# Kernel tuning notes

Hardware: AMD Instinct MI355X
Metric: run time of the kernel (lower is better)

Reference implementation:

```python
import jax, jax.numpy as jnp
import numpy as np
from jax import lax

DIM = 8          # per-head dim
HEADS = 32       # in_channels // dim * heads_ratio = 256 // 8
SCALE = 5        # multi-scale aggregation kernel
EPS = 1e-15


def _conv2d(x, w, groups=1, pad=0):
    # NCHW conv, stride 1, symmetric padding, no bias
    return lax.conv_general_dilated(
        x, w, window_strides=(1, 1), padding=[(pad, pad), (pad, pad)],
        dimension_numbers=('NCHW', 'OIHW', 'NCHW'), feature_group_count=groups)


def setup_inputs() -> dict:
    key = jax.random.key(0)
    ks = jax.random.split(key, 5)
    B, C, H, W = 8, 256, 64, 64
    td = HEADS * DIM                      # total_dim = 256
    x = jax.random.normal(ks[0], (B, C, H, W), jnp.float32)
    w_qkv = jax.random.normal(ks[1], (3 * td, C, 1, 1), jnp.float32) * 0.05
    w_dw = jax.random.normal(ks[2], (3 * td, 1, SCALE, SCALE), jnp.float32) * 0.05
    w_pw = jax.random.normal(ks[3], (3 * td, (3 * td) // (3 * HEADS), 1, 1), jnp.float32) * 0.1
    w_proj = jax.random.normal(ks[4], (C, td * 2, 1, 1), jnp.float32) * 0.05
    return {'x': x, 'w_qkv': w_qkv, 'w_dw': w_dw, 'w_pw': w_pw, 'w_proj': w_proj}


def reference(x, w_qkv, w_dw, w_pw, w_proj):
    B, C, H, W = x.shape
    td = HEADS * DIM
    # qkv projection (1x1 conv, no norm/activation)
    qkv = _conv2d(x, w_qkv)                                        # [B, 3*td, H, W]
    # multi-scale aggregation: depthwise 5x5 then grouped 1x1 (groups = 3*heads)
    agg = _conv2d(qkv, w_dw, groups=3 * td, pad=SCALE // 2)        # depthwise
    agg = _conv2d(agg, w_pw, groups=3 * HEADS)                     # grouped pointwise
    ms = jnp.concatenate([qkv, agg], axis=1)                       # [B, 2*3*td, H, W]
    # reshape to head-groups: [B, G, N, 3*dim] with G = 2*heads, N = H*W
    ms = ms.reshape(B, -1, 3 * DIM, H * W).transpose(0, 1, 3, 2)
    q, k, v = jnp.split(ms, 3, axis=-1)                            # each [B, G, N, d]
    q = jax.nn.relu(q)
    k = jax.nn.relu(k)
    v = jnp.pad(v, ((0, 0), (0, 0), (0, 0), (0, 1)), constant_values=1.0)  # [B,G,N,d+1]
    # linear attention in fp32 (inputs already fp32)
    kv = jnp.einsum('bgnd,bgne->bgde', k, v)                       # [B,G,d,d+1]
    out = jnp.einsum('bgnd,bgde->bgne', q, kv)                     # [B,G,N,d+1]
    out = out[..., :-1] / (out[..., -1:] + EPS)                    # [B,G,N,d]
    out = out.transpose(0, 1, 3, 2).reshape(B, -1, H, W)           # [B, 2*td, H, W]
    return _conv2d(out, w_proj)                                    # [B, C_out, H, W]
```

## Files before the change

kernel.cpp:

```cpp
#include <hip/hip_runtime.h>

#define N_PIX 4096
#define IMG_W 64
#define C_IN 256
#define TD3 768
#define N_B 8
#define N_G 64
#define C_OUT 256

typedef _Float16 f16;
typedef _Float16 half8 __attribute__((ext_vector_type(8)));
typedef _Float16 f16x4 __attribute__((ext_vector_type(4)));
typedef float f32x4 __attribute__((ext_vector_type(4)));

__global__ __launch_bounds__(256) void k_cvtw(const float* __restrict__ wq,
                                              const float* __restrict__ wp,
                                              f16* __restrict__ wqq_h,
                                              f16* __restrict__ wqq_l,
                                              f16* __restrict__ wqkv,
                                              f16* __restrict__ wph) {
  const int i = blockIdx.x * 256 + threadIdx.x;
  if (i < TD3 * C_IN) {
    const int r = i >> 8, k = i & 255;
    const float v = wq[i];
    const f16 h = (f16)v;
    const int g = r / 24, j = r % 24;
    if (j < 8) {
      const int qi = g * 8 + j;
      wqq_h[qi * 256 + k] = h;
      wqq_l[qi * 256 + k] = (f16)(v - (float)h);
    } else {
      const int kvi = g * 16 + (j - 8);
      wqkv[kvi * 256 + k] = h;
    }
  } else if (i < TD3 * C_IN + C_OUT * 512) {
    const int j = i - TD3 * C_IN;
    wph[j] = (f16)wp[j];
  }
}

__global__ __launch_bounds__(256) void k_xT(const float* __restrict__ x,
                                            f16* __restrict__ xh,
                                            f16* __restrict__ xl) {
  __shared__ float st[64][65];
  const int t = threadIdx.x;
  const int n0 = blockIdx.x * 64;
  const int k0 = blockIdx.y * 64;
  const size_t b = blockIdx.z;
  const float* xb = x + b * (size_t)C_IN * N_PIX;
#pragma unroll
  for (int i = 0; i < 16; ++i) {
    const int idx = t + i * 256;
    const int r = idx >> 6, c = idx & 63;
    st[r][c] = xb[(size_t)(k0 + r) * N_PIX + n0 + c];
  }
  __syncthreads();
#pragma unroll
  for (int i = 0; i < 16; ++i) {
    const int idx = t + i * 256;
    const int n = idx >> 6, k = idx & 63;
    const float v = st[k][n];
    const f16 h = (f16)v;
    const size_t o = (b * N_PIX + n0 + n) * C_IN + k0 + k;
    xh[o] = h;
    xl[o] = (f16)(v - (float)h);
  }
}

__global__ __launch_bounds__(256) void k_gemmq(const f16* __restrict__ Ah,
                                               const f16* __restrict__ Al,
                                               const f16* __restrict__ Bh,
                                               const f16* __restrict__ Bl,
                                               f16* __restrict__ C,
                                               int M, int K) {
  __shared__ f16 sm[2][32 * 512];
  const int t = threadIdx.x;
  const int lane = t & 63;
  const int w = t >> 6;

  const int per = gridDim.x >> 3;
  const int swz = (blockIdx.x & 7) * per + (blockIdx.x >> 3);
  const int mtiles = M >> 7;
  const int mt = swz % mtiles;
  const int rest = swz / mtiles;
  const int nt = rest & 31;
  const size_t bz = rest >> 5;
  const int m0 = mt * 128;
  const int n0 = nt * 128;

  const f16* Bhb = Bh + bz * (size_t)N_PIX * K;
  const f16* Blb = Bl + bz * (size_t)N_PIX * K;
  f16* Cb = C + bz * (size_t)TD3 * N_PIX;

  f32x4 acc[4][4];
#pragma unroll
  for (int i = 0; i < 4; ++i)
#pragma unroll
    for (int j = 0; j < 4; ++j) acc[i][j] = (f32x4){0.f, 0.f, 0.f, 0.f};

  const int wm = w >> 1, wn = w & 1;
  const int fr = lane & 15;
  const int fk = (lane >> 4) * 8;

  const f16* gsrc[8];
  int sslot[8];
#pragma unroll
  for (int i = 0; i < 8; ++i) {
    const int s = w + i * 4;
    const int frag = s & 7;
    const f16* base;
    int row0;
    if (s < 8) {
      base = Ah; row0 = m0;
    } else if (s < 16) {
      base = Al; row0 = m0;
    } else if (s < 24) {
      base = Bhb; row0 = n0;
    } else {
      base = Blb; row0 = n0;
    }
    gsrc[i] = base + (size_t)(row0 + frag * 16 + fr) * K + fk;
    sslot[i] = s * 512;
  }

#pragma unroll
  for (int i = 0; i < 8; ++i)
    __builtin_amdgcn_global_load_lds(
        (const __attribute__((address_space(1))) unsigned int*)gsrc[i],
        (__attribute__((address_space(3))) unsigned int*)&sm[0][sslot[i]], 16, 0, 0);

  const int ntk = K / 32;
  int cur = 0;
  for (int tt = 0; tt < ntk; ++tt) {
    if (tt + 1 < ntk) {
#pragma unroll
      for (int i = 0; i < 8; ++i)
        __builtin_amdgcn_global_load_lds(
            (const __attribute__((address_space(1))) unsigned int*)(gsrc[i] + (tt + 1) * 32),
            (__attribute__((address_space(3))) unsigned int*)&sm[cur ^ 1][sslot[i]], 16, 0, 0);
      asm volatile("s_waitcnt vmcnt(8)" ::: "memory");
    } else {
      asm volatile("s_waitcnt vmcnt(0)" ::: "memory");
    }
    __builtin_amdgcn_s_barrier();
    const f16* smb = sm[cur];
    half8 ah[4], al[4], bh[4], bl[4];
#pragma unroll
    for (int mi = 0; mi < 4; ++mi) {
      ah[mi] = *(const half8*)&smb[(wm * 4 + mi) * 512 + lane * 8];
      al[mi] = *(const half8*)&smb[(8 + wm * 4 + mi) * 512 + lane * 8];
    }
#pragma unroll
    for (int ni = 0; ni < 4; ++ni) {
      bh[ni] = *(const half8*)&smb[(16 + wn * 4 + ni) * 512 + lane * 8];
      bl[ni] = *(const half8*)&smb[(24 + wn * 4 + ni) * 512 + lane * 8];
    }
#pragma unroll
    for (int mi = 0; mi < 4; ++mi)
#pragma unroll
      for (int ni = 0; ni < 4; ++ni) {
        acc[mi][ni] = __builtin_amdgcn_mfma_f32_16x16x32_f16(ah[mi], bh[ni], acc[mi][ni], 0, 0, 0);
        acc[mi][ni] = __builtin_amdgcn_mfma_f32_16x16x32_f16(ah[mi], bl[ni], acc[mi][ni], 0, 0, 0);
        acc[mi][ni] = __builtin_amdgcn_mfma_f32_16x16x32_f16(al[mi], bh[ni], acc[mi][ni], 0, 0, 0);
      }
    __builtin_amdgcn_s_barrier();
    cur ^= 1;
  }
  const int cr = (lane >> 4) * 4;
  const int cc = lane & 15;
#pragma unroll
  for (int mi = 0; mi < 4; ++mi)
#pragma unroll
    for (int ni = 0; ni < 4; ++ni) {
#pragma unroll
      for (int r = 0; r < 4; ++r) {
        const int row = m0 + wm * 64 + mi * 16 + cr + r;
        const int ch = (row >> 3) * 24 + (row & 7);
        Cb[(size_t)ch * N_PIX + n0 + wn * 64 + ni * 16 + cc] = (f16)acc[mi][ni][r];
      }
    }
}

__global__ __launch_bounds__(256) void k_gemmkv(const f16* __restrict__ A,
                                                const f16* __restrict__ B,
                                                f16* __restrict__ C,
                                                int M, int K) {
  __shared__ f16 sm[2][16 * 1024];
  const int t = threadIdx.x;
  const int lane = t & 63;
  const int w = t >> 6;

  const int per = gridDim.x >> 3;
  const int swz = (blockIdx.x & 7) * per + (blockIdx.x >> 3);
  const int mtiles = M >> 7;
  const int mt = swz % mtiles;
  const int rest = swz / mtiles;
  const int nt = rest & 31;
  const size_t bz = rest >> 5;
  const int m0 = mt * 128;
  const int n0 = nt * 128;

  const f16* Bb = B + bz * (size_t)N_PIX * K;
  f16* Cb = C + bz * (size_t)TD3 * N_PIX;

  f32x4 acc[4][4];
#pragma unroll
  for (int i = 0; i < 4; ++i)
#pragma unroll
    for (int j = 0; j < 4; ++j) acc[i][j] = (f32x4){0.f, 0.f, 0.f, 0.f};

  const int wm = w >> 1, wn = w & 1;
  const int fr2 = lane >> 3;
  const int fko = (lane & 7) * 8;
  const f16* gsrc[4][2];
  int sslot[4][2];
#pragma unroll
  for (int i = 0; i < 4; ++i) {
    const int s = w + i * 4;
    const int frag = s & 7;
    const f16* base = (s < 8) ? A : Bb;
    const int row0 = (s < 8) ? m0 : n0;
#pragma unroll
    for (int j = 0; j < 2; ++j) {
      gsrc[i][j] = base + (size_t)(row0 + frag * 16 + j * 8 + fr2) * K + fko;
      sslot[i][j] = s * 1024 + j * 512;
    }
  }

#pragma unroll
  for (int i = 0; i < 4; ++i)
#pragma unroll
    for (int j = 0; j < 2; ++j)
      __builtin_amdgcn_global_load_lds(
          (const __attribute__((address_space(1))) unsigned int*)gsrc[i][j],
          (__attribute__((address_space(3))) unsigned int*)&sm[0][sslot[i][j]], 16, 0, 0);

  const int ntk = K / 64;
  int cur = 0;
  for (int tt = 0; tt < ntk; ++tt) {
    if (tt + 1 < ntk) {
#pragma unroll
      for (int i = 0; i < 4; ++i)
#pragma unroll
        for (int j = 0; j < 2; ++j)
          __builtin_amdgcn_global_load_lds(
              (const __attribute__((address_space(1))) unsigned int*)(gsrc[i][j] + (tt + 1) * 64),
              (__attribute__((address_space(3))) unsigned int*)&sm[cur ^ 1][sslot[i][j]], 16, 0, 0);
      asm volatile("s_waitcnt vmcnt(8)" ::: "memory");
    } else {
      asm volatile("s_waitcnt vmcnt(0)" ::: "memory");
    }
    __builtin_amdgcn_s_barrier();
    const f16* smb = sm[cur];
    const int fb = (lane & 15) * 64 + (lane >> 4) * 8;
    half8 av[4][2], bv[4][2];
#pragma unroll
    for (int mi = 0; mi < 4; ++mi)
#pragma unroll
      for (int kk = 0; kk < 2; ++kk)
        av[mi][kk] = *(const half8*)&smb[(wm * 4 + mi) * 1024 + fb + kk * 32];
#pragma unroll
    for (int ni = 0; ni < 4; ++ni)
#pragma unroll
      for (int kk = 0; kk < 2; ++kk)
        bv[ni][kk] = *(const half8*)&smb[(8 + wn * 4 + ni) * 1024 + fb + kk * 32];
#pragma unroll
    for (int kk = 0; kk < 2; ++kk)
#pragma unroll
      for (int mi = 0; mi < 4; ++mi)
#pragma unroll
        for (int ni = 0; ni < 4; ++ni)
          acc[mi][ni] = __builtin_amdgcn_mfma_f32_16x16x32_f16(av[mi][kk], bv[ni][kk], acc[mi][ni], 0, 0, 0);
    __builtin_amdgcn_s_barrier();
    cur ^= 1;
  }
  const int cr = (lane >> 4) * 4;
  const int cc = lane & 15;
#pragma unroll
  for (int mi = 0; mi < 4; ++mi)
#pragma unroll
    for (int ni = 0; ni < 4; ++ni) {
#pragma unroll
      for (int r = 0; r < 4; ++r) {
        const int row = m0 + wm * 64 + mi * 16 + cr + r;
        const int ch = (row >> 4) * 24 + 8 + (row & 15);
        Cb[(size_t)ch * N_PIX + n0 + wn * 64 + ni * 16 + cc] = (f16)acc[mi][ni][r];
      }
    }
}

template <typename OutT>
__global__ __launch_bounds__(256) void k_gemm1(const f16* __restrict__ A,
                                               const f16* __restrict__ B,
                                               OutT* __restrict__ C,
                                               int M, int K) {
  __shared__ f16 sm[2][16 * 512];
  const int t = threadIdx.x;
  const int lane = t & 63;
  const int w = t >> 6;
  const int n0 = blockIdx.x * 128;
  const int m0 = blockIdx.y * 128;
  const size_t bz = blockIdx.z;
  const f16* Bb = B + bz * (size_t)N_PIX * K;
  OutT* Cb = C + bz * (size_t)M * N_PIX;

  f32x4 acc[4][4];
#pragma unroll
  for (int i = 0; i < 4; ++i)
#pragma unroll
    for (int j = 0; j < 4; ++j) acc[i][j] = (f32x4){0.f, 0.f, 0.f, 0.f};

  const int wm = w >> 1, wn = w & 1;
  const int fr = lane & 15;
  const int fk = (lane >> 4) * 8;

  const f16* gsrc[4];
  int sslot[4];
#pragma unroll
  for (int i = 0; i < 4; ++i) {
    const int s = w + i * 4;
    const int frag = s & 7;
    const f16* base;
    int row0;
    if (s < 8) {
      base = A; row0 = m0;
    } else {
      base = Bb; row0 = n0;
    }
    gsrc[i] = base + (size_t)(row0 + frag * 16 + fr) * K + fk;
    sslot[i] = s * 512;
  }

#pragma unroll
  for (int i = 0; i < 4; ++i)
    __builtin_amdgcn_global_load_lds(
        (const __attribute__((address_space(1))) unsigned int*)gsrc[i],
        (__attribute__((address_space(3))) unsigned int*)&sm[0][sslot[i]], 16, 0, 0);

  const int nt = K / 32;
  int cur = 0;
  for (int tt = 0; tt < nt; ++tt) {
    if (tt + 1 < nt) {
#pragma unroll
      for (int i = 0; i < 4; ++i)
        __builtin_amdgcn_global_load_lds(
            (const __attribute__((address_space(1))) unsigned int*)(gsrc[i] + (tt + 1) * 32),
            (__attribute__((address_space(3))) unsigned int*)&sm[cur ^ 1][sslot[i]], 16, 0, 0);
      asm volatile("s_waitcnt vmcnt(4)" ::: "memory");
    } else {
      asm volatile("s_waitcnt vmcnt(0)" ::: "memory");
    }
    __builtin_amdgcn_s_barrier();
    const f16* smb = sm[cur];
    half8 av[4], bv[4];
#pragma unroll
    for (int mi = 0; mi < 4; ++mi) av[mi] = *(const half8*)&smb[(wm * 4 + mi) * 512 + lane * 8];
#pragma unroll
    for (int ni = 0; ni < 4; ++ni) bv[ni] = *(const half8*)&smb[(8 + wn * 4 + ni) * 512 + lane * 8];
#pragma unroll
    for (int mi = 0; mi < 4; ++mi)
#pragma unroll
      for (int ni = 0; ni < 4; ++ni)
        acc[mi][ni] = __builtin_amdgcn_mfma_f32_16x16x32_f16(av[mi], bv[ni], acc[mi][ni], 0, 0, 0);
    __builtin_amdgcn_s_barrier();
    cur ^= 1;
  }
  const int cr = (lane >> 4) * 4;
  const int cc = lane & 15;
#pragma unroll
  for (int mi = 0; mi < 4; ++mi)
#pragma unroll
    for (int ni = 0; ni < 4; ++ni) {
      OutT* p = Cb + (size_t)(m0 + wm * 64 + mi * 16 + cr) * N_PIX + n0 + wn * 64 + ni * 16 + cc;
#pragma unroll
      for (int r = 0; r < 4; ++r) p[(size_t)r * N_PIX] = (OutT)acc[mi][ni][r];
    }
}

__global__ __launch_bounds__(256) void k_dw(const f16* __restrict__ qkv,
                                            const float* __restrict__ wdw,
                                            f16* __restrict__ dw) {
  __shared__ float sin_[68][72];
  const int t = threadIdx.x;
  const int bc = blockIdx.x;
  const int ch = bc % TD3;
  const f16* src = qkv + (size_t)bc * N_PIX;

  for (int i = t; i < 68 * 72 / 4; i += 256) ((f32x4*)sin_)[i] = (f32x4){0.f, 0.f, 0.f, 0.f};
  float wreg[25];
#pragma unroll
  for (int i = 0; i < 25; ++i) wreg[i] = wdw[(size_t)ch * 25 + i];
  __syncthreads();
  for (int i = t; i < 512; i += 256) {
    const int r = i >> 3, c8 = (i & 7) * 8;
    const half8 p = *(const half8*)(src + r * 64 + c8);
    f32x4 lo = {(float)p[0], (float)p[1], (float)p[2], (float)p[3]};
    f32x4 hi = {(float)p[4], (float)p[5], (float)p[6], (float)p[7]};
    *(f32x4*)&sin_[r + 2][c8 + 4] = lo;
    *(f32x4*)&sin_[r + 2][c8 + 8] = hi;
  }
  __syncthreads();

  const int c = t & 63;
  const int rg = t >> 6;
  const int r0 = rg * 16;
  float win[5][5];
#pragma unroll
  for (int r = 0; r < 4; ++r)
#pragma unroll
    for (int j = 0; j < 5; ++j) win[r][j] = sin_[r0 + r][c + 2 + j];
#pragma unroll
  for (int orow = 0; orow < 16; ++orow) {
    const int slot = (orow + 4) % 5;
#pragma unroll
    for (int j = 0; j < 5; ++j) win[slot][j] = sin_[r0 + orow + 4][c + 2 + j];
    float s = 0.f;
#pragma unroll
    for (int dr = 0; dr < 5; ++dr) {
      const int rs = (orow + dr) % 5;
#pragma unroll
      for (int dc = 0; dc < 5; ++dc) s = fmaf(win[rs][dc], wreg[dr * 5 + dc], s);
    }
    dw[(size_t)bc * N_PIX + (r0 + orow) * 64 + c] = (f16)s;
  }
}

__global__ __launch_bounds__(256) void k_pw(const f16* __restrict__ dw,
                                            const float* __restrict__ wpw,
                                            f16* __restrict__ agg) {
  const int t = threadIdx.x;
  const int q = blockIdx.x;
  const int bg = blockIdx.y;
  const int g = bg % 96;
  float wp[64];
#pragma unroll
  for (int i = 0; i < 64; ++i) wp[i] = wpw[(size_t)g * 64 + i];
  const size_t base = ((size_t)(bg / 96) * TD3 + g * 8) * N_PIX + q * 1024;
  const int px0 = t * 4;
  float dv[8][4];
#pragma unroll
  for (int ic = 0; ic < 8; ++ic) {
    const f16x4 v = *(const f16x4*)(dw + base + (size_t)ic * N_PIX + px0);
#pragma unroll
    for (int j = 0; j < 4; ++j) dv[ic][j] = (float)v[j];
  }
#pragma unroll
  for (int oc = 0; oc < 8; ++oc) {
    f16x4 o;
#pragma unroll
    for (int j = 0; j < 4; ++j) {
      float s = 0.f;
#pragma unroll
      for (int ic = 0; ic < 8; ++ic) s = fmaf(dv[ic][j], wp[oc * 8 + ic], s);
      o[j] = (f16)s;
    }
    *(f16x4*)(agg + base + (size_t)oc * N_PIX + px0) = o;
  }
}

__global__ __launch_bounds__(256, 1) void k_kv(const f16* __restrict__ qkv,
                                               const f16* __restrict__ agg,
                                               float* __restrict__ kvbuf) {
  const int t = threadIdx.x;
  const int g = blockIdx.x;
  const int b = blockIdx.y;
  const f16* src = (g < 32) ? qkv : agg;
  const int base = (g & 31) * 24;
  const f16* kc = src + ((size_t)b * TD3 + base + 8) * N_PIX;
  const f16* vc = src + ((size_t)b * TD3 + base + 16) * N_PIX;

  float acc[72];
#pragma unroll
  for (int i = 0; i < 72; i++) acc[i] = 0.f;

  for (int i = 0; i < N_PIX / 256; i++) {
    const int n = t + i * 256;
    float kd[8], ve[8];
#pragma unroll
    for (int d = 0; d < 8; d++) kd[d] = fmaxf((float)kc[(size_t)d * N_PIX + n], 0.f);
#pragma unroll
    for (int e = 0; e < 8; e++) ve[e] = (float)vc[(size_t)e * N_PIX + n];
#pragma unroll
    for (int d = 0; d < 8; d++) {
#pragma unroll
      for (int e = 0; e < 8; e++) acc[d * 9 + e] = fmaf(kd[d], ve[e], acc[d * 9 + e]);
      acc[d * 9 + 8] += kd[d];
    }
  }

  const int lane = t & 63, wv = t >> 6;
#pragma unroll
  for (int i = 0; i < 72; i++) acc[i] += __shfl_xor(acc[i], 32, 64);
  const int hi = lane >> 5;
  float r[36];
#pragma unroll
  for (int i = 0; i < 36; i++) r[i] = hi ? acc[36 + i] : acc[i];
#pragma unroll
  for (int off = 16; off >= 1; off >>= 1) {
#pragma unroll
    for (int i = 0; i < 36; i++) r[i] += __shfl_xor(r[i], off, 64);
  }
  __shared__ float red[4][72];
  if (lane == 0 || lane == 32) {
#pragma unroll
    for (int i = 0; i < 36; i++) red[wv][hi * 36 + i] = r[i];
  }
  __syncthreads();
  if (t < 72) {
    const float s = red[0][t] + red[1][t] + red[2][t] + red[3][t];
    kvbuf[((size_t)b * N_G + g) * 72 + t] = s;
  }
}

__global__ __launch_bounds__(256) void k_att(const f16* __restrict__ qkvh,
                                             const f16* __restrict__ aggh,
                                             const float* __restrict__ kvbuf,
                                             f16* __restrict__ atth) {
  __shared__ float skv[N_G * 72];
  __shared__ f16 sa[512][34];
  const int t = threadIdx.x;
  const int n0 = blockIdx.x * 32;
  const size_t b = blockIdx.y;
  for (int i = t; i < N_G * 72; i += 256) skv[i] = kvbuf[b * (N_G * 72) + i];
  __syncthreads();
  const int px = t & 31, gq = t >> 5;
#pragma unroll
  for (int gi = 0; gi < 8; ++gi) {
    const int g = gq * 8 + gi;
    const f16* src = (g < 32) ? qkvh : aggh;
    const int base = (g & 31) * 24;
    const f16* qc = src + ((size_t)b * TD3 + base) * N_PIX + n0 + px;
    float num[8] = {0.f, 0.f, 0.f, 0.f, 0.f, 0.f, 0.f, 0.f};
    float den = 0.f;
#pragma unroll
    for (int d = 0; d < 8; ++d) {
      const float qd = fmaxf((float)qc[(size_t)d * N_PIX], 0.f);
      const float* kvg = &skv[g * 72 + d * 9];
#pragma unroll
      for (int e = 0; e < 8; ++e) num[e] = fmaf(qd, kvg[e], num[e]);
      den = fmaf(qd, kvg[8], den);
    }
    const float rd = 1.f / (den + 1e-15f);
#pragma unroll
    for (int e = 0; e < 8; ++e) sa[g * 8 + e][px] = (f16)(num[e] * rd);
  }
  __syncthreads();
  f16* dst = atth + (b * N_PIX + n0) * 512;
  for (int i = 0; i < 64; ++i) {
    const int idx = t + i * 256;
    dst[idx] = sa[idx & 511][idx >> 9];
  }
}

extern "C" void kernel_launch(void* const* d_in, const int* in_sizes, int n_in,
                              void* d_out, int out_size, void* d_ws, size_t ws_size,
                              hipStream_t stream) {
  const float* x = (const float*)d_in[0];
  const float* w_qkv = (const float*)d_in[1];
  const float* w_dw = (const float*)d_in[2];
  const float* w_pw = (const float*)d_in[3];
  const float* w_proj = (const float*)d_in[4];
  float* out = (float*)d_out;

  char* ws = (char*)d_ws;
  size_t off = 0;
  f16* qkvh = (f16*)(ws + off); off += (size_t)N_B * TD3 * N_PIX * 2;
  f16* aggh = (f16*)(ws + off); off += (size_t)N_B * TD3 * N_PIX * 2;
  float* kvbuf = (float*)(ws + off); off += (size_t)N_B * N_G * 72 * 4;
  f16* wqq_h = (f16*)(ws + off); off += (size_t)256 * C_IN * 2;
  f16* wqq_l = (f16*)(ws + off); off += (size_t)256 * C_IN * 2;
  f16* wqkv = (f16*)(ws + off); off += (size_t)512 * C_IN * 2;
  f16* wph = (f16*)(ws + off); off += (size_t)C_OUT * 512 * 2;
  f16* xTh = (f16*)(ws + off);
  f16* xTl = xTh + (size_t)N_B * N_PIX * C_IN;
  f16* dwbuf = (f16*)(ws + off);
  f16* atth = (f16*)(ws + off);

  const int ncvt = (TD3 * C_IN + C_OUT * 512 + 255) / 256;
  k_cvtw<<<dim3(ncvt), 256, 0, stream>>>(w_qkv, w_proj, wqq_h, wqq_l, wqkv, wph);
  k_xT<<<dim3(N_PIX / 64, C_IN / 64, N_B), 256, 0, stream>>>(x, xTh, xTl);
  k_gemmq<<<dim3(2 * 32 * N_B), 256, 0, stream>>>(
      wqq_h, wqq_l, xTh, xTl, qkvh, 256, C_IN);
  k_gemmkv<<<dim3(4 * 32 * N_B), 256, 0, stream>>>(
      wqkv, xTh, qkvh, 512, C_IN);
  k_dw<<<dim3(N_B * TD3), 256, 0, stream>>>(qkvh, w_dw, dwbuf);
  k_pw<<<dim3(4, N_B * 96), 256, 0, stream>>>(dwbuf, w_pw, aggh);
  k_kv<<<dim3(N_G, N_B), 256, 0, stream>>>(qkvh, aggh, kvbuf);
  k_att<<<dim3(N_PIX / 32, N_B), 256, 0, stream>>>(qkvh, aggh, kvbuf, atth);
  k_gemm1<float><<<dim3(N_PIX / 128, C_OUT / 128, N_B), 256, 0, stream>>>(
      wph, atth, out, C_OUT, 512);
}
```

Before: 158.2 us.

## Fuse attention output with projection GEMM in one kernel

The attention kernel now keeps its 32-pixel by 512-channel fp16 tile in shared memory and directly computes the output projection with MFMA, writing the final fp32 output. This removes the atth intermediate buffer round trip and the separate GEMM launch. In exchange, each block reloads the whole 256x512 projection weight from global memory (cached in L2) without LDS staging, and uses a small 32-pixel N tile, which may reduce MFMA efficiency compared with the 128x128 tiled GEMM.

```diff
diff --git a/kernel.cpp b/kernel.cpp
--- a/kernel.cpp
+++ b/kernel.cpp
@@ -289,94 +289,6 @@
     }
 }
 
-template <typename OutT>
-__global__ __launch_bounds__(256) void k_gemm1(const f16* __restrict__ A,
-                                               const f16* __restrict__ B,
-                                               OutT* __restrict__ C,
-                                               int M, int K) {
-  __shared__ f16 sm[2][16 * 512];
-  const int t = threadIdx.x;
-  const int lane = t & 63;
-  const int w = t >> 6;
-  const int n0 = blockIdx.x * 128;
-  const int m0 = blockIdx.y * 128;
-  const size_t bz = blockIdx.z;
-  const f16* Bb = B + bz * (size_t)N_PIX * K;
-  OutT* Cb = C + bz * (size_t)M * N_PIX;
-
-  f32x4 acc[4][4];
-#pragma unroll
-  for (int i = 0; i < 4; ++i)
-#pragma unroll
-    for (int j = 0; j < 4; ++j) acc[i][j] = (f32x4){0.f, 0.f, 0.f, 0.f};
-
-  const int wm = w >> 1, wn = w & 1;
-  const int fr = lane & 15;
-  const int fk = (lane >> 4) * 8;
-
-  const f16* gsrc[4];
-  int sslot[4];
-#pragma unroll
-  for (int i = 0; i < 4; ++i) {
-    const int s = w + i * 4;
-    const int frag = s & 7;
-    const f16* base;
-    int row0;
-    if (s < 8) {
-      base = A; row0 = m0;
-    } else {
-      base = Bb; row0 = n0;
-    }
-    gsrc[i] = base + (size_t)(row0 + frag * 16 + fr) * K + fk;
-    sslot[i] = s * 512;
-  }
-
-#pragma unroll
-  for (int i = 0; i < 4; ++i)
-    __builtin_amdgcn_global_load_lds(
-        (const __attribute__((address_space(1))) unsigned int*)gsrc[i],
-        (__attribute__((address_space(3))) unsigned int*)&sm[0][sslot[i]], 16, 0, 0);
-
-  const int nt = K / 32;
-  int cur = 0;
-  for (int tt = 0; tt < nt; ++tt) {
-    if (tt + 1 < nt) {
-#pragma unroll
-      for (int i = 0; i < 4; ++i)
-        __builtin_amdgcn_global_load_lds(
-            (const __attribute__((address_space(1))) unsigned int*)(gsrc[i] + (tt + 1) * 32),
-            (__attribute__((address_space(3))) unsigned int*)&sm[cur ^ 1][sslot[i]], 16, 0, 0);
-      asm volatile("s_waitcnt vmcnt(4)" ::: "memory");
-    } else {
-      asm volatile("s_waitcnt vmcnt(0)" ::: "memory");
-    }
-    __builtin_amdgcn_s_barrier();
-    const f16* smb = sm[cur];
-    half8 av[4], bv[4];
-#pragma unroll
-    for (int mi = 0; mi < 4; ++mi) av[mi] = *(const half8*)&smb[(wm * 4 + mi) * 512 + lane * 8];
-#pragma unroll
-    for (int ni = 0; ni < 4; ++ni) bv[ni] = *(const half8*)&smb[(8 + wn * 4 + ni) * 512 + lane * 8];
-#pragma unroll
-    for (int mi = 0; mi < 4; ++mi)
-#pragma unroll
-      for (int ni = 0; ni < 4; ++ni)
-        acc[mi][ni] = __builtin_amdgcn_mfma_f32_16x16x32_f16(av[mi], bv[ni], acc[mi][ni], 0, 0, 0);
-    __builtin_amdgcn_s_barrier();
-    cur ^= 1;
-  }
-  const int cr = (lane >> 4) * 4;
-  const int cc = lane & 15;
-#pragma unroll
-  for (int mi = 0; mi < 4; ++mi)
-#pragma unroll
-    for (int ni = 0; ni < 4; ++ni) {
-      OutT* p = Cb + (size_t)(m0 + wm * 64 + mi * 16 + cr) * N_PIX + n0 + wn * 64 + ni * 16 + cc;
-#pragma unroll
-      for (int r = 0; r < 4; ++r) p[(size_t)r * N_PIX] = (OutT)acc[mi][ni][r];
-    }
-}
-
 __global__ __launch_bounds__(256) void k_dw(const f16* __restrict__ qkv,
                                             const float* __restrict__ wdw,
                                             f16* __restrict__ dw) {
@@ -512,12 +424,13 @@
   }
 }
 
-__global__ __launch_bounds__(256) void k_att(const f16* __restrict__ qkvh,
-                                             const f16* __restrict__ aggh,
-                                             const float* __restrict__ kvbuf,
-                                             f16* __restrict__ atth) {
+__global__ __launch_bounds__(256) void k_attproj(const f16* __restrict__ qkvh,
+                                                 const f16* __restrict__ aggh,
+                                                 const float* __restrict__ kvbuf,
+                                                 const f16* __restrict__ wph,
+                                                 float* __restrict__ out) {
   __shared__ float skv[N_G * 72];
-  __shared__ f16 sa[512][34];
+  __shared__ f16 sa2[32][520];
   const int t = threadIdx.x;
   const int n0 = blockIdx.x * 32;
   const size_t b = blockIdx.y;
@@ -541,15 +454,48 @@
       den = fmaf(qd, kvg[8], den);
     }
     const float rd = 1.f / (den + 1e-15f);
-#pragma unroll
-    for (int e = 0; e < 8; ++e) sa[g * 8 + e][px] = (f16)(num[e] * rd);
+    half8 o;
+#pragma unroll
+    for (int e = 0; e < 8; ++e) o[e] = (f16)(num[e] * rd);
+    *(half8*)&sa2[px][g * 8] = o;
   }
   __syncthreads();
-  f16* dst = atth + (b * N_PIX + n0) * 512;
-  for (int i = 0; i < 64; ++i) {
-    const int idx = t + i * 256;
-    dst[idx] = sa[idx & 511][idx >> 9];
-  }
+
+  const int lane = t & 63;
+  const int w = t >> 6;
+  const int fr = lane & 15;
+  const int fko = (lane >> 4) * 8;
+  f32x4 acc[4][2];
+#pragma unroll
+  for (int i = 0; i < 4; ++i)
+#pragma unroll
+    for (int j = 0; j < 2; ++j) acc[i][j] = (f32x4){0.f, 0.f, 0.f, 0.f};
+
+#pragma unroll 4
+  for (int kc = 0; kc < 16; ++kc) {
+    half8 a[4], bf[2];
+#pragma unroll
+    for (int mi = 0; mi < 4; ++mi)
+      a[mi] = *(const half8*)(wph + (size_t)(w * 64 + mi * 16 + fr) * 512 + kc * 32 + fko);
+#pragma unroll
+    for (int ni = 0; ni < 2; ++ni)
+      bf[ni] = *(const half8*)&sa2[ni * 16 + fr][kc * 32 + fko];
+#pragma unroll
+    for (int mi = 0; mi < 4; ++mi)
+#pragma unroll
+      for (int ni = 0; ni < 2; ++ni)
+        acc[mi][ni] = __builtin_amdgcn_mfma_f32_16x16x32_f16(a[mi], bf[ni], acc[mi][ni], 0, 0, 0);
+  }
+  const int cr = (lane >> 4) * 4;
+  const int cc = lane & 15;
+  float* ob = out + b * (size_t)C_OUT * N_PIX;
+#pragma unroll
+  for (int mi = 0; mi < 4; ++mi)
+#pragma unroll
+    for (int ni = 0; ni < 2; ++ni)
+#pragma unroll
+      for (int r = 0; r < 4; ++r)
+        ob[(size_t)(w * 64 + mi * 16 + cr + r) * N_PIX + n0 + ni * 16 + cc] = acc[mi][ni][r];
 }
 
 extern "C" void kernel_launch(void* const* d_in, const int* in_sizes, int n_in,
@@ -574,7 +520,6 @@
   f16* xTh = (f16*)(ws + off);
   f16* xTl = xTh + (size_t)N_B * N_PIX * C_IN;
   f16* dwbuf = (f16*)(ws + off);
-  f16* atth = (f16*)(ws + off);
 
   const int ncvt = (TD3 * C_IN + C_OUT * 512 + 255) / 256;
   k_cvtw<<<dim3(ncvt), 256, 0, stream>>>(w_qkv, w_proj, wqq_h, wqq_l, wqkv, wph);
@@ -586,7 +531,6 @@
   k_dw<<<dim3(N_B * TD3), 256, 0, stream>>>(qkvh, w_dw, dwbuf);
   k_pw<<<dim3(4, N_B * 96), 256, 0, stream>>>(dwbuf, w_pw, aggh);
   k_kv<<<dim3(N_G, N_B), 256, 0, stream>>>(qkvh, aggh, kvbuf);
-  k_att<<<dim3(N_PIX / 32, N_B), 256, 0, stream>>>(qkvh, aggh, kvbuf, atth);
-  k_gemm1<float><<<dim3(N_PIX / 128, C_OUT / 128, N_B), 256, 0, stream>>>(
-      wph, atth, out, C_OUT, 512);
-}
+  k_attproj<<<dim3(N_PIX / 32, N_B), 256, 0, stream>>>(
+      qkvh, aggh, kvbuf, wph, out);
+}
```

New measurement: 171.5 us. +8.4%, slower.

## Deepen output GEMM K-tile, swizzle its grid, vectorize x transpose stores

Applied to the files above, without the earlier changes.

The final projection GEMM now stages 64-wide K slices per iteration instead of 32, which halves the number of barrier/wait rounds and doubles the MFMA work per sync. It also uses a 1-D grid with an XCD-aware swizzle so that tiles sharing data land on the same chiplet. Separately, the x transpose kernel writes pairs of f16 values per store instead of single halves. The trade-off is twice the LDS use per block in the GEMM, which may cut occupancy.

```diff
diff --git a/kernel.cpp b/kernel.cpp
--- a/kernel.cpp
+++ b/kernel.cpp
@@ -11,6 +11,7 @@
 typedef _Float16 f16;
 typedef _Float16 half8 __attribute__((ext_vector_type(8)));
 typedef _Float16 f16x4 __attribute__((ext_vector_type(4)));
+typedef _Float16 f16x2 __attribute__((ext_vector_type(2)));
 typedef float f32x4 __attribute__((ext_vector_type(4)));
 
 __global__ __launch_bounds__(256) void k_cvtw(const float* __restrict__ wq,
@@ -56,14 +57,14 @@
   }
   __syncthreads();
 #pragma unroll
-  for (int i = 0; i < 16; ++i) {
+  for (int i = 0; i < 8; ++i) {
     const int idx = t + i * 256;
-    const int n = idx >> 6, k = idx & 63;
-    const float v = st[k][n];
-    const f16 h = (f16)v;
-    const size_t o = (b * N_PIX + n0 + n) * C_IN + k0 + k;
-    xh[o] = h;
-    xl[o] = (f16)(v - (float)h);
+    const int n = idx >> 5, k2 = (idx & 31) * 2;
+    const float v0 = st[k2][n], v1 = st[k2 + 1][n];
+    const f16 h0 = (f16)v0, h1 = (f16)v1;
+    const size_t o = (b * N_PIX + n0 + n) * C_IN + k0 + k2;
+    *(f16x2*)(xh + o) = (f16x2){h0, h1};
+    *(f16x2*)(xl + o) = (f16x2){(f16)(v0 - (float)h0), (f16)(v1 - (float)h1)};
   }
 }
 
@@ -289,20 +290,27 @@
     }
 }
 
-template <typename OutT>
 __global__ __launch_bounds__(256) void k_gemm1(const f16* __restrict__ A,
                                                const f16* __restrict__ B,
-                                               OutT* __restrict__ C,
+                                               float* __restrict__ C,
                                                int M, int K) {
-  __shared__ f16 sm[2][16 * 512];
+  __shared__ f16 sm[2][16 * 1024];
   const int t = threadIdx.x;
   const int lane = t & 63;
   const int w = t >> 6;
-  const int n0 = blockIdx.x * 128;
-  const int m0 = blockIdx.y * 128;
-  const size_t bz = blockIdx.z;
+
+  const int per = gridDim.x >> 3;
+  const int swz = (blockIdx.x & 7) * per + (blockIdx.x >> 3);
+  const int mtiles = M >> 7;
+  const int mt = swz % mtiles;
+  const int rest = swz / mtiles;
+  const int nt = rest & 31;
+  const size_t bz = rest >> 5;
+  const int m0 = mt * 128;
+  const int n0 = nt * 128;
+
   const f16* Bb = B + bz * (size_t)N_PIX * K;
-  OutT* Cb = C + bz * (size_t)M * N_PIX;
+  float* Cb = C + bz * (size_t)M * N_PIX;
 
   f32x4 acc[4][4];
 #pragma unroll
@@ -311,57 +319,67 @@
     for (int j = 0; j < 4; ++j) acc[i][j] = (f32x4){0.f, 0.f, 0.f, 0.f};
 
   const int wm = w >> 1, wn = w & 1;
-  const int fr = lane & 15;
-  const int fk = (lane >> 4) * 8;
-
-  const f16* gsrc[4];
-  int sslot[4];
+  const int fr2 = lane >> 3;
+  const int fko = (lane & 7) * 8;
+  const f16* gsrc[4][2];
+  int sslot[4][2];
 #pragma unroll
   for (int i = 0; i < 4; ++i) {
     const int s = w + i * 4;
     const int frag = s & 7;
-    const f16* base;
-    int row0;
-    if (s < 8) {
-      base = A; row0 = m0;
-    } else {
-      base = Bb; row0 = n0;
-    }
-    gsrc[i] = base + (size_t)(row0 + frag * 16 + fr) * K + fk;
-    sslot[i] = s * 512;
+    const f16* base = (s < 8) ? A : Bb;
+    const int row0 = (s < 8) ? m0 : n0;
+#pragma unroll
+    for (int j = 0; j < 2; ++j) {
+      gsrc[i][j] = base + (size_t)(row0 + frag * 16 + j * 8 + fr2) * K + fko;
+      sslot[i][j] = s * 1024 + j * 512;
+    }
   }
 
 #pragma unroll
   for (int i = 0; i < 4; ++i)
-    __builtin_amdgcn_global_load_lds(
-        (const __attribute__((address_space(1))) unsigned int*)gsrc[i],
-        (__attribute__((address_space(3))) unsigned int*)&sm[0][sslot[i]], 16, 0, 0);
-
-  const int nt = K / 32;
+#pragma unroll
+    for (int j = 0; j < 2; ++j)
+      __builtin_amdgcn_global_load_lds(
+          (const __attribute__((address_space(1))) unsigned int*)gsrc[i][j],
+          (__attribute__((address_space(3))) unsigned int*)&sm[0][sslot[i][j]], 16, 0, 0);
+
+  const int ntk = K / 64;
   int cur = 0;
-  for (int tt = 0; tt < nt; ++tt) {
-    if (tt + 1 < nt) {
+  for (int tt = 0; tt < ntk; ++tt) {
+    if (tt + 1 < ntk) {
 #pragma unroll
       for (int i = 0; i < 4; ++i)
-        __builtin_amdgcn_global_load_lds(
-            (const __attribute__((address_space(1))) unsigned int*)(gsrc[i] + (tt + 1) * 32),
-            (__attribute__((address_space(3))) unsigned int*)&sm[cur ^ 1][sslot[i]], 16, 0, 0);
-      asm volatile("s_waitcnt vmcnt(4)" ::: "memory");
+#pragma unroll
+        for (int j = 0; j < 2; ++j)
+          __builtin_amdgcn_global_load_lds(
+              (const __attribute__((address_space(1))) unsigned int*)(gsrc[i][j] + (tt + 1) * 64),
+              (__attribute__((address_space(3))) unsigned int*)&sm[cur ^ 1][sslot[i][j]], 16, 0, 0);
+      asm volatile("s_waitcnt vmcnt(8)" ::: "memory");
     } else {
       asm volatile("s_waitcnt vmcnt(0)" ::: "memory");
     }
     __builtin_amdgcn_s_barrier();
     const f16* smb = sm[cur];
-    half8 av[4], bv[4];
-#pragma unroll
-    for (int mi = 0; mi < 4; ++mi) av[mi] = *(const half8*)&smb[(wm * 4 + mi) * 512 + lane * 8];
-#pragma unroll
-    for (int ni = 0; ni < 4; ++ni) bv[ni] = *(const half8*)&smb[(8 + wn * 4 + ni) * 512 + lane * 8];
+    const int fb = (lane & 15) * 64 + (lane >> 4) * 8;
+    half8 av[4][2], bv[4][2];
 #pragma unroll
     for (int mi = 0; mi < 4; ++mi)
 #pragma unroll
-      for (int ni = 0; ni < 4; ++ni)
-        acc[mi][ni] = __builtin_amdgcn_mfma_f32_16x16x32_f16(av[mi], bv[ni], acc[mi][ni], 0, 0, 0);
+      for (int kk = 0; kk < 2; ++kk)
+        av[mi][kk] = *(const half8*)&smb[(wm * 4 + mi) * 1024 + fb + kk * 32];
+#pragma unroll
+    for (int ni = 0; ni < 4; ++ni)
+#pragma unroll
+      for (int kk = 0; kk < 2; ++kk)
+        bv[ni][kk] = *(const half8*)&smb[(8 + wn * 4 + ni) * 1024 + fb + kk * 32];
+#pragma unroll
+    for (int kk = 0; kk < 2; ++kk)
+#pragma unroll
+      for (int mi = 0; mi < 4; ++mi)
+#pragma unroll
+        for (int ni = 0; ni < 4; ++ni)
+          acc[mi][ni] = __builtin_amdgcn_mfma_f32_16x16x32_f16(av[mi][kk], bv[ni][kk], acc[mi][ni], 0, 0, 0);
     __builtin_amdgcn_s_barrier();
     cur ^= 1;
   }
@@ -371,9 +389,9 @@
   for (int mi = 0; mi < 4; ++mi)
 #pragma unroll
     for (int ni = 0; ni < 4; ++ni) {
-      OutT* p = Cb + (size_t)(m0 + wm * 64 + mi * 16 + cr) * N_PIX + n0 + wn * 64 + ni * 16 + cc;
-#pragma unroll
-      for (int r = 0; r < 4; ++r) p[(size_t)r * N_PIX] = (OutT)acc[mi][ni][r];
+      float* p = Cb + (size_t)(m0 + wm * 64 + mi * 16 + cr) * N_PIX + n0 + wn * 64 + ni * 16 + cc;
+#pragma unroll
+      for (int r = 0; r < 4; ++r) p[(size_t)r * N_PIX] = acc[mi][ni][r];
     }
 }
 
@@ -587,6 +605,5 @@
   k_pw<<<dim3(4, N_B * 96), 256, 0, stream>>>(dwbuf, w_pw, aggh);
   k_kv<<<dim3(N_G, N_B), 256, 0, stream>>>(qkvh, aggh, kvbuf);
   k_att<<<dim3(N_PIX / 32, N_B), 256, 0, stream>>>(qkvh, aggh, kvbuf, atth);
-  k_gemm1<float><<<dim3(N_PIX / 128, C_OUT / 128, N_B), 256, 0, stream>>>(
-      wph, atth, out, C_OUT, 512);
-}
+  k_gemm1<<<dim3(2 * 32 * N_B), 256, 0, stream>>>(wph, atth, out, C_OUT, 512);
+}
```

After: 152.9 us. 1.03x faster.
